# Kernel tuning notes

Hardware: AMD Instinct MI355X
Metric: run time of the kernel (lower is better)

Reference implementation:

```python
import jax, jax.numpy as jnp
import numpy as np

H = 64  # hidden_dimension
F = 8   # number_of_input_features
P = 64  # prediction_length
B = 1024
T = 512


def _lstm_cell(x, h, c, Wih, Whh, bih, bhh):
    # PyTorch gate order: input, forget, cell(g), output
    gates = x @ Wih.T + h @ Whh.T + (bih + bhh)  # [B, 4H]
    i, f, g, o = jnp.split(gates, 4, axis=-1)
    c_new = jax.nn.sigmoid(f) * c + jax.nn.sigmoid(i) * jnp.tanh(g)
    h_new = jax.nn.sigmoid(o) * jnp.tanh(c_new)
    return h_new, c_new


def setup_inputs() -> dict:
    key = jax.random.key(0)
    ks = jax.random.split(key, 11)
    s = 1.0 / np.sqrt(H)
    u = lambda k, shape: jax.random.uniform(k, shape, jnp.float32, -s, s)
    return {
        "input_sequence": jax.random.normal(ks[0], (B, T, F), jnp.float32),
        "enc_Wih": u(ks[1], (4 * H, F)),
        "enc_Whh": u(ks[2], (4 * H, H)),
        "enc_bih": u(ks[3], (4 * H,)),
        "enc_bhh": u(ks[4], (4 * H,)),
        "dec_Wih": u(ks[5], (4 * H, F)),
        "dec_Whh": u(ks[6], (4 * H, H)),
        "dec_bih": u(ks[7], (4 * H,)),
        "dec_bhh": u(ks[8], (4 * H,)),
        "fc_W": u(ks[9], (F, H)),
        "fc_b": u(ks[10], (F,)),
    }


def reference(input_sequence, enc_Wih, enc_Whh, enc_bih, enc_bhh,
              dec_Wih, dec_Whh, dec_bih, dec_bhh, fc_W, fc_b):
    Bn = input_sequence.shape[0]
    h0 = jnp.zeros((Bn, H), input_sequence.dtype)
    c0 = jnp.zeros((Bn, H), input_sequence.dtype)

    # ---- Encoder: scan over time ----
    xs = jnp.swapaxes(input_sequence, 0, 1)  # [T, B, F]

    def enc_step(carry, x_t):
        h, c = carry
        h, c = _lstm_cell(x_t, h, c, enc_Wih, enc_Whh, enc_bih, enc_bhh)
        return (h, c), None

    (h, c), _ = jax.lax.scan(enc_step, (h0, c0), xs)

    x_last = input_sequence[:, -1, :]  # [B, F]

    def dec_step(carry, _):
        h, c, x = carry
        h, c = _lstm_cell(x, h, c, dec_Wih, dec_Whh, dec_bih, dec_bhh)
        pred = h @ fc_W.T + fc_b  # [B, F]
        return (h, c, pred), pred

    _, preds = jax.lax.scan(dec_step, (h, c, x_last), None, length=P)
    return jnp.swapaxes(preds, 0, 1)  # [B, P, F]
```

## Files before the change

kernel.cpp:

```cpp
#include <hip/hip_runtime.h>


#define Hh 64
#define Ff 8
#define Tt 512
#define Pp 64
#define BATCH 1024
#define MB 4
#define NBLK (BATCH / MB)
#define ROWS 72
#define ABUF (16 * ROWS + 64)
#define XSTRIDE 32

typedef __attribute__((ext_vector_type(8))) _Float16 half8;
typedef __attribute__((ext_vector_type(4))) _Float16 half4;
typedef __attribute__((ext_vector_type(4))) float f32x4;

#define LOG2E  1.44269504088896340736f
#define K2LOG2 2.88538008177792681472f

__device__ __forceinline__ float rcp_(float x)  { return __builtin_amdgcn_rcpf(x); }
__device__ __forceinline__ float exp2_(float x) { return __builtin_amdgcn_exp2f(x); }
__device__ __forceinline__ int arow_base(int m) { return m * ROWS + (m & 3) * 16; }

__device__ __forceinline__ void load_wfrags(
    const float* __restrict__ Whh, const float* __restrict__ Wih,
    int wv, int q, int col, half8 w0[4], half8 w1[4], half8 wx[4])
{
    #pragma unroll
    for (int Tg = 0; Tg < 4; ++Tg) {
        int g = Tg * 64 + wv * 16 + col;
        float sc = (Tg == 2) ? K2LOG2 : LOG2E;
        const float* r0 = Whh + g * 64 + q * 8;
        #pragma unroll
        for (int j = 0; j < 8; ++j) {
            w0[Tg][j] = (_Float16)(r0[j] * sc);
            w1[Tg][j] = (_Float16)(r0[32 + j] * sc);
            wx[Tg][j] = (q == 0) ? (_Float16)(Wih[g * 8 + j] * sc) : (_Float16)0.f;
        }
    }
}

__device__ __forceinline__ void pchain(half8 ax, const half8 wx[4],
                                       const f32x4 biasv[4], f32x4 P[4])
{
    P[2] = __builtin_amdgcn_mfma_f32_16x16x32_f16(ax, wx[2], biasv[2], 0, 0, 0);
    P[0] = __builtin_amdgcn_mfma_f32_16x16x32_f16(ax, wx[0], biasv[0], 0, 0, 0);
    P[1] = __builtin_amdgcn_mfma_f32_16x16x32_f16(ax, wx[1], biasv[1], 0, 0, 0);
    P[3] = __builtin_amdgcn_mfma_f32_16x16x32_f16(ax, wx[3], biasv[3], 0, 0, 0);
}

__device__ __forceinline__ float qcell(half8 a0, half8 a1,
    const half8 w0[4], const half8 w1[4], const f32x4 P[4], float& cS)
{
    f32x4 Qg = __builtin_amdgcn_mfma_f32_16x16x32_f16(a0, w0[2], P[2], 0, 0, 0);
    f32x4 Qi = __builtin_amdgcn_mfma_f32_16x16x32_f16(a0, w0[0], P[0], 0, 0, 0);
    f32x4 Qf = __builtin_amdgcn_mfma_f32_16x16x32_f16(a0, w0[1], P[1], 0, 0, 0);
    f32x4 Qo = __builtin_amdgcn_mfma_f32_16x16x32_f16(a0, w0[3], P[3], 0, 0, 0);
    Qg = __builtin_amdgcn_mfma_f32_16x16x32_f16(a1, w1[2], Qg, 0, 0, 0);
    Qi = __builtin_amdgcn_mfma_f32_16x16x32_f16(a1, w1[0], Qi, 0, 0, 0);
    Qf = __builtin_amdgcn_mfma_f32_16x16x32_f16(a1, w1[1], Qf, 0, 0, 0);
    Qo = __builtin_amdgcn_mfma_f32_16x16x32_f16(a1, w1[3], Qo, 0, 0, 0);

    float eg = exp2_(Qg[0]);
    float ei = exp2_(-Qi[0]);
    float ef = exp2_(-Qf[0]);
    float eo = exp2_(-Qo[0]);
    float it = (eg - 1.f) * rcp_((1.f + ei) * (1.f + eg));
    float sf = rcp_(1.f + ef);
    cS = __builtin_fmaf(sf, cS, K2LOG2 * it);
    float cc = fminf(fmaxf(cS, -60.f), 60.f);
    float ec = exp2_(cc);
    return (ec - 1.f) * rcp_((1.f + eo) * (1.f + ec));
}

__global__ __launch_bounds__(256, 1)
void seq2seq_v12(const float* __restrict__ x_seq,
                 const float* __restrict__ eWih, const float* __restrict__ eWhh,
                 const float* __restrict__ ebih, const float* __restrict__ ebhh,
                 const float* __restrict__ dWih, const float* __restrict__ dWhh,
                 const float* __restrict__ dbih, const float* __restrict__ dbhh,
                 const float* __restrict__ fcW,  const float* __restrict__ fcb,
                 float* __restrict__ out)
{
    __shared__ __align__(16) _Float16 xs[(Tt + 2) * XSTRIDE];
    __shared__ __align__(16) _Float16 A0[ABUF];
    __shared__ __align__(16) _Float16 A1[ABUF];

    const int tid  = threadIdx.x;
    const int wv   = tid >> 6;
    const int lane = tid & 63;
    const int q    = lane >> 4;
    const int col  = lane & 15;
    const int u    = wv * 16 + col;
    const int b0   = blockIdx.x * MB;

    half8 w0[4], w1[4], wx[4];
    load_wfrags(eWhh, eWih, wv, q, col, w0, w1, wx);
    f32x4 biasv[4];
    #pragma unroll
    for (int Tg = 0; Tg < 4; ++Tg) {
        int g = Tg * 64 + u;
        float sc = (Tg == 2) ? K2LOG2 : LOG2E;
        float bv = (ebih[g] + ebhh[g]) * sc;
        biasv[Tg] = (f32x4){bv, bv, bv, bv};
    }

    { int* Z0 = (int*)A0; int* Z1 = (int*)A1;
      for (int i = tid; i < ABUF / 2; i += 256) { Z0[i] = 0; Z1[i] = 0; } }
    if (tid < 32) ((int*)xs)[Tt * 16 + tid] = 0;
    for (int i = tid; i < MB * Tt * 2; i += 256) {
        int b   = i >> 10;
        int rem = i & 1023;
        int t   = rem >> 1;
        int f4  = (rem & 1) * 4;
        const float* src = x_seq + ((size_t)(b0 + b) * Tt + t) * Ff + f4;
        half4 s = { (_Float16)src[0], (_Float16)src[1], (_Float16)src[2], (_Float16)src[3] };
        *(half4*)(&xs[t * XSTRIDE + b * 8 + f4]) = s;
    }
    __syncthreads();

    const _Float16* arA = A0 + arow_base(col) + q * 8;
    const _Float16* arB = A1 + arow_base(col) + q * 8;
    _Float16* hwA = A0 + 4 * q * ROWS + u;
    _Float16* hwB = A1 + 4 * q * ROWS + u;
    const _Float16* xq = xs + (col >> 2) * 8;

    float cS = 0.f;
    f32x4 P[4];
    {   half8 ax = *(const half8*)(xq);
        pchain(ax, wx, biasv, P);
        xq += XSTRIDE; }

    for (int t = 0; t < Tt; t += 2) {
        __syncthreads();
        {
            half8 ax = *(const half8*)(xq); xq += XSTRIDE;
            half8 a0 = *(const half8*)(arA);
            half8 a1 = *(const half8*)(arA + 32);
            float hn = qcell(a0, a1, w0, w1, P, cS);
            *hwB = (_Float16)hn;
            pchain(ax, wx, biasv, P);
        }
        __syncthreads();
        {
            half8 ax = *(const half8*)(xq); xq += XSTRIDE;
            half8 a0 = *(const half8*)(arB);
            half8 a1 = *(const half8*)(arB + 32);
            float hn = qcell(a0, a1, w0, w1, P, cS);
            *hwA = (_Float16)hn;
            pchain(ax, wx, biasv, P);
        }
    }

    half8 axl = *(const half8*)(xs + (Tt - 1) * XSTRIDE + (col >> 2) * 8);

    half8 wp0[4], wp1[4];
    f32x4 biasp[4];
    #pragma unroll
    for (int Tg = 0; Tg < 4; ++Tg) {
        int g = Tg * 64 + u;
        float sc = (Tg == 2) ? K2LOG2 : LOG2E;
        #pragma unroll
        for (int j = 0; j < 8; ++j) {
            int k0 = q * 8 + j;
            float v0 = dWhh[g * 64 + k0];
            float v1 = dWhh[g * 64 + 32 + k0];
            w0[Tg][j] = (_Float16)(v0 * sc);
            w1[Tg][j] = (_Float16)(v1 * sc);
            wx[Tg][j] = (q == 0) ? (_Float16)(dWih[g * 8 + j] * sc) : (_Float16)0.f;
            float s0 = v0, s1 = v1;
            #pragma unroll
            for (int f = 0; f < 8; ++f) {
                float wif = dWih[g * 8 + f];
                s0 = __builtin_fmaf(wif, fcW[f * 64 + k0], s0);
                s1 = __builtin_fmaf(wif, fcW[f * 64 + 32 + k0], s1);
            }
            wp0[Tg][j] = (_Float16)(s0 * sc);
            wp1[Tg][j] = (_Float16)(s1 * sc);
        }
        float bb = dbih[g] + dbhh[g];
        float bp = bb;
        #pragma unroll
        for (int f = 0; f < 8; ++f) bp = __builtin_fmaf(dWih[g * 8 + f], fcb[f], bp);
        biasv[Tg] = (f32x4){bb * sc, bb * sc, bb * sc, bb * sc};
        biasp[Tg] = (f32x4){bp * sc, bp * sc, bp * sc, bp * sc};
    }
    half8 wf0, wf1;
    f32x4 biasf;
    {
        #pragma unroll
        for (int j = 0; j < 8; ++j) {
            wf0[j] = (col < 8) ? (_Float16)fcW[col * 64 + q * 8 + j]      : (_Float16)0.f;
            wf1[j] = (col < 8) ? (_Float16)fcW[col * 64 + 32 + q * 8 + j] : (_Float16)0.f;
        }
        float fb = (col < 8) ? fcb[col] : 0.f;
        biasf = (f32x4){fb, fb, fb, fb};
    }

    float* predbuf = (float*)xs;
    const bool pw = (wv == 0) && (col < 8);

    __syncthreads();
    {
        half8 a0 = *(const half8*)(arA);
        half8 a1 = *(const half8*)(arA + 32);
        pchain(axl, wx, biasv, P);
        float hn = qcell(a0, a1, w0, w1, P, cS);
        *hwB = (_Float16)hn;
    }

    for (int p = 1; p < Pp; ++p) {
        __syncthreads();
        const _Float16* ar = (p & 1) ? arB : arA;
        _Float16*       hw = (p & 1) ? hwA : hwB;
        half8 a0 = *(const half8*)(ar);
        half8 a1 = *(const half8*)(ar + 32);
        float hn = qcell(a0, a1, wp0, wp1, biasp, cS);
        *hw = (_Float16)hn;
        f32x4 F = __builtin_amdgcn_mfma_f32_16x16x32_f16(a0, wf0, biasf, 0, 0, 0);
        F       = __builtin_amdgcn_mfma_f32_16x16x32_f16(a1, wf1, F,     0, 0, 0);
        if (pw) predbuf[q * (Pp * Ff) + (p - 1) * Ff + col] = F[0];
    }

    __syncthreads();
    {
        half8 a0 = *(const half8*)(arA);
        half8 a1 = *(const half8*)(arA + 32);
        f32x4 F = __builtin_amdgcn_mfma_f32_16x16x32_f16(a0, wf0, biasf, 0, 0, 0);
        F       = __builtin_amdgcn_mfma_f32_16x16x32_f16(a1, wf1, F,     0, 0, 0);
        if (pw) predbuf[q * (Pp * Ff) + (Pp - 1) * Ff + col] = F[0];
    }
    __syncthreads();

    {
        f32x4* out4 = (f32x4*)out + (size_t)b0 * (Pp * Ff / 4);
        const f32x4* pb4 = (const f32x4*)predbuf;
        for (int i = tid; i < MB * Pp * Ff / 4; i += 256)
            out4[i] = pb4[i];
    }
}

extern "C" void kernel_launch(void* const* d_in, const int* in_sizes, int n_in,
                              void* d_out, int out_size, void* d_ws, size_t ws_size,
                              hipStream_t stream) {
    (void)in_sizes; (void)n_in; (void)d_ws; (void)ws_size; (void)out_size;
    hipLaunchKernelGGL(seq2seq_v12, dim3(NBLK), dim3(256), 0, stream,
                       (const float*)d_in[0],
                       (const float*)d_in[1], (const float*)d_in[2],
                       (const float*)d_in[3], (const float*)d_in[4],
                       (const float*)d_in[5], (const float*)d_in[6],
                       (const float*)d_in[7], (const float*)d_in[8],
                       (const float*)d_in[9], (const float*)d_in[10],
                       (float*)d_out);
}
```

Before: 219.2 us.

## Reorder LSTM step to overlap next input projection with gate math and swizzle LDS

Splits the cell into a gate-MFMA phase and an activation phase. The next step's input-projection MFMA chain and the FC projection are issued before the transcendental math so they overlap the serial critical path. The output activation is rewritten as sigmoid(o)*(1-2/(1+e^2c)) using fmed3 and one fewer multiply in the dependent chain. The hidden-state LDS write and read addresses are XOR-swizzled by quad to reduce bank conflicts, which depends on the read and write permutations matching.

```diff
diff --git a/kernel.cpp b/kernel.cpp
--- a/kernel.cpp
+++ b/kernel.cpp
@@ -50,32 +50,38 @@
     P[3] = __builtin_amdgcn_mfma_f32_16x16x32_f16(ax, wx[3], biasv[3], 0, 0, 0);
 }
 
-__device__ __forceinline__ float qcell(half8 a0, half8 a1,
-    const half8 w0[4], const half8 w1[4], const f32x4 P[4], float& cS)
-{
-    f32x4 Qg = __builtin_amdgcn_mfma_f32_16x16x32_f16(a0, w0[2], P[2], 0, 0, 0);
-    f32x4 Qi = __builtin_amdgcn_mfma_f32_16x16x32_f16(a0, w0[0], P[0], 0, 0, 0);
-    f32x4 Qf = __builtin_amdgcn_mfma_f32_16x16x32_f16(a0, w0[1], P[1], 0, 0, 0);
-    f32x4 Qo = __builtin_amdgcn_mfma_f32_16x16x32_f16(a0, w0[3], P[3], 0, 0, 0);
-    Qg = __builtin_amdgcn_mfma_f32_16x16x32_f16(a1, w1[2], Qg, 0, 0, 0);
-    Qi = __builtin_amdgcn_mfma_f32_16x16x32_f16(a1, w1[0], Qi, 0, 0, 0);
-    Qf = __builtin_amdgcn_mfma_f32_16x16x32_f16(a1, w1[1], Qf, 0, 0, 0);
-    Qo = __builtin_amdgcn_mfma_f32_16x16x32_f16(a1, w1[3], Qo, 0, 0, 0);
-
-    float eg = exp2_(Qg[0]);
-    float ei = exp2_(-Qi[0]);
-    float ef = exp2_(-Qf[0]);
-    float eo = exp2_(-Qo[0]);
+__device__ __forceinline__ void qgates(half8 a0, half8 a1,
+    const half8 w0[4], const half8 w1[4], const f32x4 P[4], f32x4 Q[4])
+{
+    Q[2] = __builtin_amdgcn_mfma_f32_16x16x32_f16(a0, w0[2], P[2], 0, 0, 0);
+    Q[2] = __builtin_amdgcn_mfma_f32_16x16x32_f16(a1, w1[2], Q[2], 0, 0, 0);
+    Q[0] = __builtin_amdgcn_mfma_f32_16x16x32_f16(a0, w0[0], P[0], 0, 0, 0);
+    Q[0] = __builtin_amdgcn_mfma_f32_16x16x32_f16(a1, w1[0], Q[0], 0, 0, 0);
+    Q[1] = __builtin_amdgcn_mfma_f32_16x16x32_f16(a0, w0[1], P[1], 0, 0, 0);
+    Q[1] = __builtin_amdgcn_mfma_f32_16x16x32_f16(a1, w1[1], Q[1], 0, 0, 0);
+    Q[3] = __builtin_amdgcn_mfma_f32_16x16x32_f16(a0, w0[3], P[3], 0, 0, 0);
+    Q[3] = __builtin_amdgcn_mfma_f32_16x16x32_f16(a1, w1[3], Q[3], 0, 0, 0);
+}
+
+__device__ __forceinline__ float cellf(const f32x4 Q[4], float& cS)
+{
+    float eg = exp2_(Q[2][0]);
+    float ei = exp2_(-Q[0][0]);
     float it = (eg - 1.f) * rcp_((1.f + ei) * (1.f + eg));
+    float ef = exp2_(-Q[1][0]);
     float sf = rcp_(1.f + ef);
+    float eo = exp2_(-Q[3][0]);
+    float so   = rcp_(1.f + eo);
+    float m2so = -2.f * so;
     cS = __builtin_fmaf(sf, cS, K2LOG2 * it);
-    float cc = fminf(fmaxf(cS, -60.f), 60.f);
+    float cc = __builtin_amdgcn_fmed3f(cS, -60.f, 60.f);
     float ec = exp2_(cc);
-    return (ec - 1.f) * rcp_((1.f + eo) * (1.f + ec));
+    float rc = rcp_(1.f + ec);
+    return __builtin_fmaf(m2so, rc, so);
 }
 
 __global__ __launch_bounds__(256, 1)
-void seq2seq_v12(const float* __restrict__ x_seq,
+void seq2seq_v13(const float* __restrict__ x_seq,
                  const float* __restrict__ eWih, const float* __restrict__ eWhh,
                  const float* __restrict__ ebih, const float* __restrict__ ebhh,
                  const float* __restrict__ dWih, const float* __restrict__ dWhh,
@@ -120,10 +126,12 @@
     }
     __syncthreads();
 
-    const _Float16* arA = A0 + arow_base(col) + q * 8;
-    const _Float16* arB = A1 + arow_base(col) + q * 8;
-    _Float16* hwA = A0 + 4 * q * ROWS + u;
-    _Float16* hwB = A1 + 4 * q * ROWS + u;
+    const int qr = (col & 8) ? (q ^ 2) : q;
+    const _Float16* arA = A0 + arow_base(col) + qr * 8;
+    const _Float16* arB = A1 + arow_base(col) + qr * 8;
+    const int uw = u ^ ((q & 2) << 3);
+    _Float16* hwA = A0 + 4 * q * ROWS + uw;
+    _Float16* hwB = A1 + 4 * q * ROWS + uw;
     const _Float16* xq = xs + (col >> 2) * 8;
 
     float cS = 0.f;
@@ -135,21 +143,25 @@
     for (int t = 0; t < Tt; t += 2) {
         __syncthreads();
         {
-            half8 ax = *(const half8*)(xq); xq += XSTRIDE;
             half8 a0 = *(const half8*)(arA);
             half8 a1 = *(const half8*)(arA + 32);
-            float hn = qcell(a0, a1, w0, w1, P, cS);
+            half8 ax = *(const half8*)(xq); xq += XSTRIDE;
+            f32x4 Q[4];
+            qgates(a0, a1, w0, w1, P, Q);
+            pchain(ax, wx, biasv, P);
+            float hn = cellf(Q, cS);
             *hwB = (_Float16)hn;
-            pchain(ax, wx, biasv, P);
         }
         __syncthreads();
         {
-            half8 ax = *(const half8*)(xq); xq += XSTRIDE;
             half8 a0 = *(const half8*)(arB);
             half8 a1 = *(const half8*)(arB + 32);
-            float hn = qcell(a0, a1, w0, w1, P, cS);
+            half8 ax = *(const half8*)(xq); xq += XSTRIDE;
+            f32x4 Q[4];
+            qgates(a0, a1, w0, w1, P, Q);
+            pchain(ax, wx, biasv, P);
+            float hn = cellf(Q, cS);
             *hwA = (_Float16)hn;
-            pchain(ax, wx, biasv, P);
         }
     }
 
@@ -201,12 +213,14 @@
     float* predbuf = (float*)xs;
     const bool pw = (wv == 0) && (col < 8);
 
+    pchain(axl, wx, biasv, P);
     __syncthreads();
     {
         half8 a0 = *(const half8*)(arA);
         half8 a1 = *(const half8*)(arA + 32);
-        pchain(axl, wx, biasv, P);
-        float hn = qcell(a0, a1, w0, w1, P, cS);
+        f32x4 Q[4];
+        qgates(a0, a1, w0, w1, P, Q);
+        float hn = cellf(Q, cS);
         *hwB = (_Float16)hn;
     }
 
@@ -216,10 +230,12 @@
         _Float16*       hw = (p & 1) ? hwA : hwB;
         half8 a0 = *(const half8*)(ar);
         half8 a1 = *(const half8*)(ar + 32);
-        float hn = qcell(a0, a1, wp0, wp1, biasp, cS);
-        *hw = (_Float16)hn;
+        f32x4 Q[4];
+        qgates(a0, a1, wp0, wp1, biasp, Q);
         f32x4 F = __builtin_amdgcn_mfma_f32_16x16x32_f16(a0, wf0, biasf, 0, 0, 0);
         F       = __builtin_amdgcn_mfma_f32_16x16x32_f16(a1, wf1, F,     0, 0, 0);
+        float hn = cellf(Q, cS);
+        *hw = (_Float16)hn;
         if (pw) predbuf[q * (Pp * Ff) + (p - 1) * Ff + col] = F[0];
     }
 
@@ -245,7 +261,7 @@
                               void* d_out, int out_size, void* d_ws, size_t ws_size,
                               hipStream_t stream) {
     (void)in_sizes; (void)n_in; (void)d_ws; (void)ws_size; (void)out_size;
-    hipLaunchKernelGGL(seq2seq_v12, dim3(NBLK), dim3(256), 0, stream,
+    hipLaunchKernelGGL(seq2seq_v13, dim3(NBLK), dim3(256), 0, stream,
                        (const float*)d_in[0],
                        (const float*)d_in[1], (const float*)d_in[2],
                        (const float*)d_in[3], (const float*)d_in[4],
```

After: 223.8 us. +2.1%, slower.

## Split gate MFMA chains, pack input projection into one MFMA, retune LDS padding

Applied to the files above, without the earlier changes.

Each gate's two dependent K-halves now accumulate as independent MFMAs whose results are summed afterwards, which shortens the serial MFMA dependency chain on the recurrent critical path. The four per-gate input projections collapse into a single MFMA by packing gates into quad rows with lane-selected input, and that result is broadcast to the gate accumulators. The activation math is rewritten (fmed3 clamp, sigmoid-based tanh form), and the LDS row stride changes from 72 to 68. The trade is extra VALU adds and broadcasts, plus possible changes in LDS bank conflicts from the new padding.

```diff
diff --git a/kernel.cpp b/kernel.cpp
--- a/kernel.cpp
+++ b/kernel.cpp
@@ -8,7 +8,7 @@
 #define BATCH 1024
 #define MB 4
 #define NBLK (BATCH / MB)
-#define ROWS 72
+#define ROWS 68
 #define ABUF (16 * ROWS + 64)
 #define XSTRIDE 32
 
@@ -19,13 +19,15 @@
 #define LOG2E  1.44269504088896340736f
 #define K2LOG2 2.88538008177792681472f
 
+#define MFMA16(a, b, c) __builtin_amdgcn_mfma_f32_16x16x32_f16(a, b, c, 0, 0, 0)
+
 __device__ __forceinline__ float rcp_(float x)  { return __builtin_amdgcn_rcpf(x); }
 __device__ __forceinline__ float exp2_(float x) { return __builtin_amdgcn_exp2f(x); }
 __device__ __forceinline__ int arow_base(int m) { return m * ROWS + (m & 3) * 16; }
 
 __device__ __forceinline__ void load_wfrags(
-    const float* __restrict__ Whh, const float* __restrict__ Wih,
-    int wv, int q, int col, half8 w0[4], half8 w1[4], half8 wx[4])
+    const float* __restrict__ Whh, int wv, int q, int col,
+    half8 w0[4], half8 w1[4])
 {
     #pragma unroll
     for (int Tg = 0; Tg < 4; ++Tg) {
@@ -36,46 +38,48 @@
         for (int j = 0; j < 8; ++j) {
             w0[Tg][j] = (_Float16)(r0[j] * sc);
             w1[Tg][j] = (_Float16)(r0[32 + j] * sc);
-            wx[Tg][j] = (q == 0) ? (_Float16)(Wih[g * 8 + j] * sc) : (_Float16)0.f;
-        }
-    }
-}
-
-__device__ __forceinline__ void pchain(half8 ax, const half8 wx[4],
-                                       const f32x4 biasv[4], f32x4 P[4])
+        }
+    }
+}
+
+__device__ __forceinline__ void qgates2(half8 a0, half8 a1,
+    const half8 w0[4], const half8 w1[4], const f32x4 Ci[4], f32x4 Z,
+    f32x4 QA[4], f32x4 QB[4])
 {
-    P[2] = __builtin_amdgcn_mfma_f32_16x16x32_f16(ax, wx[2], biasv[2], 0, 0, 0);
-    P[0] = __builtin_amdgcn_mfma_f32_16x16x32_f16(ax, wx[0], biasv[0], 0, 0, 0);
-    P[1] = __builtin_amdgcn_mfma_f32_16x16x32_f16(ax, wx[1], biasv[1], 0, 0, 0);
-    P[3] = __builtin_amdgcn_mfma_f32_16x16x32_f16(ax, wx[3], biasv[3], 0, 0, 0);
-}
-
-__device__ __forceinline__ float qcell(half8 a0, half8 a1,
-    const half8 w0[4], const half8 w1[4], const f32x4 P[4], float& cS)
+    QA[2] = MFMA16(a0, w0[2], Ci[2]);
+    QB[2] = MFMA16(a1, w1[2], Z);
+    QA[0] = MFMA16(a0, w0[0], Ci[0]);
+    QB[0] = MFMA16(a1, w1[0], Z);
+    QA[1] = MFMA16(a0, w0[1], Ci[1]);
+    QB[1] = MFMA16(a1, w1[1], Z);
+    QA[3] = MFMA16(a0, w0[3], Ci[3]);
+    QB[3] = MFMA16(a1, w1[3], Z);
+}
+
+__device__ __forceinline__ float cellf2(const f32x4 QA[4], const f32x4 QB[4],
+                                        float& cS)
 {
-    f32x4 Qg = __builtin_amdgcn_mfma_f32_16x16x32_f16(a0, w0[2], P[2], 0, 0, 0);
-    f32x4 Qi = __builtin_amdgcn_mfma_f32_16x16x32_f16(a0, w0[0], P[0], 0, 0, 0);
-    f32x4 Qf = __builtin_amdgcn_mfma_f32_16x16x32_f16(a0, w0[1], P[1], 0, 0, 0);
-    f32x4 Qo = __builtin_amdgcn_mfma_f32_16x16x32_f16(a0, w0[3], P[3], 0, 0, 0);
-    Qg = __builtin_amdgcn_mfma_f32_16x16x32_f16(a1, w1[2], Qg, 0, 0, 0);
-    Qi = __builtin_amdgcn_mfma_f32_16x16x32_f16(a1, w1[0], Qi, 0, 0, 0);
-    Qf = __builtin_amdgcn_mfma_f32_16x16x32_f16(a1, w1[1], Qf, 0, 0, 0);
-    Qo = __builtin_amdgcn_mfma_f32_16x16x32_f16(a1, w1[3], Qo, 0, 0, 0);
-
-    float eg = exp2_(Qg[0]);
-    float ei = exp2_(-Qi[0]);
-    float ef = exp2_(-Qf[0]);
-    float eo = exp2_(-Qo[0]);
+    float gg = QA[2][0] + QB[2][0];
+    float eg = exp2_(gg);
+    float gi = QA[0][0] + QB[0][0];
+    float ei = exp2_(-gi);
     float it = (eg - 1.f) * rcp_((1.f + ei) * (1.f + eg));
+    float gf = QA[1][0] + QB[1][0];
+    float ef = exp2_(-gf);
     float sf = rcp_(1.f + ef);
+    float go = QA[3][0] + QB[3][0];
+    float eo = exp2_(-go);
+    float so   = rcp_(1.f + eo);
+    float m2so = -2.f * so;
     cS = __builtin_fmaf(sf, cS, K2LOG2 * it);
-    float cc = fminf(fmaxf(cS, -60.f), 60.f);
+    float cc = __builtin_amdgcn_fmed3f(cS, -60.f, 60.f);
     float ec = exp2_(cc);
-    return (ec - 1.f) * rcp_((1.f + eo) * (1.f + ec));
+    float rc = rcp_(1.f + ec);
+    return __builtin_fmaf(m2so, rc, so);
 }
 
 __global__ __launch_bounds__(256, 1)
-void seq2seq_v12(const float* __restrict__ x_seq,
+void seq2seq_v15(const float* __restrict__ x_seq,
                  const float* __restrict__ eWih, const float* __restrict__ eWhh,
                  const float* __restrict__ ebih, const float* __restrict__ ebhh,
                  const float* __restrict__ dWih, const float* __restrict__ dWhh,
@@ -94,17 +98,21 @@
     const int col  = lane & 15;
     const int u    = wv * 16 + col;
     const int b0   = blockIdx.x * MB;
-
-    half8 w0[4], w1[4], wx[4];
-    load_wfrags(eWhh, eWih, wv, q, col, w0, w1, wx);
-    f32x4 biasv[4];
+    const bool selq = (q == (col & 3));
+    const half8 hz = {};
+    const f32x4 Zv = {0.f, 0.f, 0.f, 0.f};
+
+    half8 w0[4], w1[4];
+    load_wfrags(eWhh, wv, q, col, w0, w1);
+
+    half8 Bx;
+    f32x4 biasC;
     #pragma unroll
-    for (int Tg = 0; Tg < 4; ++Tg) {
-        int g = Tg * 64 + u;
-        float sc = (Tg == 2) ? K2LOG2 : LOG2E;
-        float bv = (ebih[g] + ebhh[g]) * sc;
-        biasv[Tg] = (f32x4){bv, bv, bv, bv};
-    }
+    for (int j = 0; j < 8; ++j)
+        Bx[j] = (_Float16)(eWih[(q * 64 + u) * 8 + j] * ((q == 2) ? K2LOG2 : LOG2E));
+    #pragma unroll
+    for (int r = 0; r < 4; ++r)
+        biasC[r] = (ebih[r * 64 + u] + ebhh[r * 64 + u]) * ((r == 2) ? K2LOG2 : LOG2E);
 
     { int* Z0 = (int*)A0; int* Z1 = (int*)A1;
       for (int i = tid; i < ABUF / 2; i += 256) { Z0[i] = 0; Z1[i] = 0; } }
@@ -127,29 +135,48 @@
     const _Float16* xq = xs + (col >> 2) * 8;
 
     float cS = 0.f;
-    f32x4 P[4];
-    {   half8 ax = *(const half8*)(xq);
-        pchain(ax, wx, biasv, P);
+    f32x4 Ci[4];
+    {   half8 xv = *(const half8*)(xq);
+        half8 ax = selq ? xv : hz;
+        f32x4 P4 = MFMA16(ax, Bx, biasC);
+        Ci[0] = P4;
+        Ci[1] = (f32x4){P4[1], P4[1], P4[1], P4[1]};
+        Ci[2] = (f32x4){P4[2], P4[2], P4[2], P4[2]};
+        Ci[3] = (f32x4){P4[3], P4[3], P4[3], P4[3]};
         xq += XSTRIDE; }
 
     for (int t = 0; t < Tt; t += 2) {
         __syncthreads();
         {
-            half8 ax = *(const half8*)(xq); xq += XSTRIDE;
             half8 a0 = *(const half8*)(arA);
             half8 a1 = *(const half8*)(arA + 32);
-            float hn = qcell(a0, a1, w0, w1, P, cS);
+            half8 xv = *(const half8*)(xq); xq += XSTRIDE;
+            f32x4 QA[4], QB[4];
+            qgates2(a0, a1, w0, w1, Ci, Zv, QA, QB);
+            half8 ax = selq ? xv : hz;
+            f32x4 P4 = MFMA16(ax, Bx, biasC);
+            float hn = cellf2(QA, QB, cS);
+            Ci[0] = P4;
+            Ci[1] = (f32x4){P4[1], P4[1], P4[1], P4[1]};
+            Ci[2] = (f32x4){P4[2], P4[2], P4[2], P4[2]};
+            Ci[3] = (f32x4){P4[3], P4[3], P4[3], P4[3]};
             *hwB = (_Float16)hn;
-            pchain(ax, wx, biasv, P);
         }
         __syncthreads();
         {
-            half8 ax = *(const half8*)(xq); xq += XSTRIDE;
             half8 a0 = *(const half8*)(arB);
             half8 a1 = *(const half8*)(arB + 32);
-            float hn = qcell(a0, a1, w0, w1, P, cS);
+            half8 xv = *(const half8*)(xq); xq += XSTRIDE;
+            f32x4 QA[4], QB[4];
+            qgates2(a0, a1, w0, w1, Ci, Zv, QA, QB);
+            half8 ax = selq ? xv : hz;
+            f32x4 P4 = MFMA16(ax, Bx, biasC);
+            float hn = cellf2(QA, QB, cS);
+            Ci[0] = P4;
+            Ci[1] = (f32x4){P4[1], P4[1], P4[1], P4[1]};
+            Ci[2] = (f32x4){P4[2], P4[2], P4[2], P4[2]};
+            Ci[3] = (f32x4){P4[3], P4[3], P4[3], P4[3]};
             *hwA = (_Float16)hn;
-            pchain(ax, wx, biasv, P);
         }
     }
 
@@ -168,7 +195,6 @@
             float v1 = dWhh[g * 64 + 32 + k0];
             w0[Tg][j] = (_Float16)(v0 * sc);
             w1[Tg][j] = (_Float16)(v1 * sc);
-            wx[Tg][j] = (q == 0) ? (_Float16)(dWih[g * 8 + j] * sc) : (_Float16)0.f;
             float s0 = v0, s1 = v1;
             #pragma unroll
             for (int f = 0; f < 8; ++f) {
@@ -183,8 +209,15 @@
         float bp = bb;
         #pragma unroll
         for (int f = 0; f < 8; ++f) bp = __builtin_fmaf(dWih[g * 8 + f], fcb[f], bp);
-        biasv[Tg] = (f32x4){bb * sc, bb * sc, bb * sc, bb * sc};
         biasp[Tg] = (f32x4){bp * sc, bp * sc, bp * sc, bp * sc};
+    }
+    {
+        #pragma unroll
+        for (int j = 0; j < 8; ++j)
+            Bx[j] = (_Float16)(dWih[(q * 64 + u) * 8 + j] * ((q == 2) ? K2LOG2 : LOG2E));
+        #pragma unroll
+        for (int r = 0; r < 4; ++r)
+            biasC[r] = (dbih[r * 64 + u] + dbhh[r * 64 + u]) * ((r == 2) ? K2LOG2 : LOG2E);
     }
     half8 wf0, wf1;
     f32x4 biasf;
@@ -201,12 +234,21 @@
     float* predbuf = (float*)xs;
     const bool pw = (wv == 0) && (col < 8);
 
+    {
+        half8 ax = selq ? axl : hz;
+        f32x4 P4 = MFMA16(ax, Bx, biasC);
+        Ci[0] = P4;
+        Ci[1] = (f32x4){P4[1], P4[1], P4[1], P4[1]};
+        Ci[2] = (f32x4){P4[2], P4[2], P4[2], P4[2]};
+        Ci[3] = (f32x4){P4[3], P4[3], P4[3], P4[3]};
+    }
     __syncthreads();
     {
         half8 a0 = *(const half8*)(arA);
         half8 a1 = *(const half8*)(arA + 32);
-        pchain(axl, wx, biasv, P);
-        float hn = qcell(a0, a1, w0, w1, P, cS);
+        f32x4 QA[4], QB[4];
+        qgates2(a0, a1, w0, w1, Ci, Zv, QA, QB);
+        float hn = cellf2(QA, QB, cS);
         *hwB = (_Float16)hn;
     }
 
@@ -216,10 +258,12 @@
         _Float16*       hw = (p & 1) ? hwA : hwB;
         half8 a0 = *(const half8*)(ar);
         half8 a1 = *(const half8*)(ar + 32);
-        float hn = qcell(a0, a1, wp0, wp1, biasp, cS);
+        f32x4 QA[4], QB[4];
+        qgates2(a0, a1, wp0, wp1, biasp, Zv, QA, QB);
+        f32x4 F = MFMA16(a0, wf0, biasf);
+        F       = MFMA16(a1, wf1, F);
+        float hn = cellf2(QA, QB, cS);
         *hw = (_Float16)hn;
-        f32x4 F = __builtin_amdgcn_mfma_f32_16x16x32_f16(a0, wf0, biasf, 0, 0, 0);
-        F       = __builtin_amdgcn_mfma_f32_16x16x32_f16(a1, wf1, F,     0, 0, 0);
         if (pw) predbuf[q * (Pp * Ff) + (p - 1) * Ff + col] = F[0];
     }
 
@@ -227,8 +271,8 @@
     {
         half8 a0 = *(const half8*)(arA);
         half8 a1 = *(const half8*)(arA + 32);
-        f32x4 F = __builtin_amdgcn_mfma_f32_16x16x32_f16(a0, wf0, biasf, 0, 0, 0);
-        F       = __builtin_amdgcn_mfma_f32_16x16x32_f16(a1, wf1, F,     0, 0, 0);
+        f32x4 F = MFMA16(a0, wf0, biasf);
+        F       = MFMA16(a1, wf1, F);
         if (pw) predbuf[q * (Pp * Ff) + (Pp - 1) * Ff + col] = F[0];
     }
     __syncthreads();
@@ -245,7 +289,7 @@
                               void* d_out, int out_size, void* d_ws, size_t ws_size,
                               hipStream_t stream) {
     (void)in_sizes; (void)n_in; (void)d_ws; (void)ws_size; (void)out_size;
-    hipLaunchKernelGGL(seq2seq_v12, dim3(NBLK), dim3(256), 0, stream,
+    hipLaunchKernelGGL(seq2seq_v15, dim3(NBLK), dim3(256), 0, stream,
                        (const float*)d_in[0],
                        (const float*)d_in[1], (const float*)d_in[2],
                        (const float*)d_in[3], (const float*)d_in[4],
```

Measured after the change: 331.0 us. 51.0% more time.
